# Kernel tuning notes

Hardware: AMD Instinct MI355X
Metric: run time of the kernel (lower is better)

The kernel has to match this reference:

```python
import jax, jax.numpy as jnp
import numpy as np

BS, C, D = 4096, 16384, 128
POS_ALPHA, POS_DELTA = 32.0, 0.1
NEG_ALPHA, NEG_DELTA = 32.0, -0.1


def _normalize(x):
    # F.normalize(x, dim=1)
    return x / jnp.linalg.norm(x, axis=1, keepdims=True)


def _masked_lse(sims, mask, axis, use_max):
    """Faithful port of Criterion.masked_logsumexp (returns per-entry lse and the
    nonzero-entry mask that torch uses to filter before the final mean)."""
    m = sims * mask
    if use_max:
        ref = jnp.max(m, axis=axis, keepdims=True)
    else:
        ref = jnp.min(m, axis=axis, keepdims=True)
    ref = jax.lax.stop_gradient(ref)  # torch: ref_v.detach()
    # torch: nz_entries = max + min of (sims*mask); keep where nonzero
    nz = (jnp.max(m, axis=axis) + jnp.min(m, axis=axis)) != 0
    s = jnp.sum(jnp.exp(sims - ref) * mask, axis=axis)
    lse = jnp.log(jnp.where(nz, s, 1.0)) + jnp.squeeze(ref, axis=axis)
    return lse, nz


def setup_inputs() -> dict:
    key = jax.random.key(0)
    k1, k2, k3 = jax.random.split(key, 3)
    batch = jax.random.normal(k1, (BS, D), dtype=jnp.float32)
    # proxies = randn/proxy_div, init_dev=0 so no max-shift
    proxies = jax.random.normal(k2, (C, D), dtype=jnp.float32) / 8.0
    labels = jax.random.randint(k3, (BS,), 0, C)
    return {"batch": batch, "proxies": proxies, "labels": labels}


def reference(batch, proxies, labels):
    batch = _normalize(batch)          # [BS, D]
    proxies = _normalize(proxies)      # [C, D]

    pos_sims = batch @ proxies[labels].T   # [BS, BS] cosine sims to positive proxies
    sims = batch @ proxies.T               # [BS, C]

    same = (labels[:, None] == labels[None, :]).astype(batch.dtype)              # [BS, BS]
    diff = (labels[:, None] != jnp.arange(C)[None, :]).astype(batch.dtype)       # [BS, C]

    w_pos = -POS_ALPHA * (pos_sims - POS_DELTA)
    w_neg = NEG_ALPHA * (sims - NEG_DELTA)

    # mode='anchor' -> dim=0; cosine -> max=False for pos, max=True for neg
    pos_lse, pos_nz = _masked_lse(w_pos, same, axis=0, use_max=False)
    neg_lse, neg_nz = _masked_lse(w_neg, diff, axis=0, use_max=True)

    # nca_clean=False -> softplus
    pos_s = jax.nn.softplus(pos_lse)
    neg_s = jax.nn.softplus(neg_lse)

    # torch takes mean only over nz entries
    pos_mean = jnp.sum(jnp.where(pos_nz, pos_s, 0.0)) / jnp.maximum(jnp.sum(pos_nz), 1).astype(batch.dtype)
    neg_mean = jnp.sum(jnp.where(neg_nz, neg_s, 0.0)) / jnp.maximum(jnp.sum(neg_nz), 1).astype(batch.dtype)
    return pos_mean + neg_mean
```

## Files before the change

kernel.cpp:

```cpp
#include <hip/hip_runtime.h>
#include <math.h>

#define BS 4096
#define C_CLS 16384
#define D 128
#define NS 8
#define NR 8
#define KE 46.16624130844683f
#define POS_C 4.616624130844683f
#define LN2 0.69314718055994531f
#define CORR_BLOCKS 256
#define NEG_BLOCKS 512

typedef __attribute__((ext_vector_type(8))) short short8;
typedef __attribute__((ext_vector_type(4))) float f32x4;

__device__ inline float bf2f(unsigned short h) {
    return __uint_as_float(((unsigned)h) << 16);
}
__device__ inline unsigned short f2bf(float f) {
    unsigned u = __float_as_uint(f);
    u += 0x7FFF + ((u >> 16) & 1);
    return (unsigned short)(u >> 16);
}
__device__ inline float fastexp2(float x) {
    return __int_as_float((int)fmaf(x, 8388608.0f, 1064866816.0f));
}
__device__ inline float softplus(float x) {
    return fmaxf(x, 0.0f) + log1pf(__expf(-fabsf(x)));
}
__device__ inline void gload16(const void* g, void* l) {
    __builtin_amdgcn_global_load_lds((const __attribute__((address_space(1))) void*)g,
                                     (__attribute__((address_space(3))) void*)l, 16, 0, 0);
}
__device__ inline unsigned fenc(float f) {
    unsigned u = __float_as_uint(f);
    return (u & 0x80000000u) ? ~u : (u | 0x80000000u);
}
__device__ inline float fdec(unsigned k) {
    return (k & 0x80000000u) ? __uint_as_float(k ^ 0x80000000u) : __uint_as_float(~k);
}

__global__ __launch_bounds__(256) void normalize_all(const float* __restrict__ batch,
                                                     const float* __restrict__ proxies,
                                                     short* __restrict__ bbf,
                                                     short* __restrict__ pbf,
                                                     float* __restrict__ acc,
                                                     float* __restrict__ negSub,
                                                     float* __restrict__ posSum,
                                                     float* __restrict__ posCnt,
                                                     unsigned* __restrict__ posMaxK,
                                                     unsigned* __restrict__ posMinK,
                                                     int* __restrict__ counter) {
    const int sub = threadIdx.x >> 5;
    const int lane32 = threadIdx.x & 31;
    const int row = blockIdx.x * 8 + sub;
    const bool isb = row < BS;
    const float* src = isb ? batch : proxies;
    short* dst = isb ? bbf : pbf;
    const int r = isb ? row : row - BS;
    const float sc = isb ? 1.0f : KE;

    float4 v = ((const float4*)(src + (size_t)r * D))[lane32];
    float ss = v.x * v.x + v.y * v.y + v.z * v.z + v.w * v.w;
#pragma unroll
    for (int off = 16; off; off >>= 1) ss += __shfl_xor(ss, off);
    float inv = rsqrtf(ss) * sc;
    ushort4 o;
    o.x = f2bf(v.x * inv);
    o.y = f2bf(v.y * inv);
    o.z = f2bf(v.z * inv);
    o.w = f2bf(v.w * inv);
    ((ushort4*)(dst + (size_t)r * D))[lane32] = o;

    const int bid = blockIdx.x, t = threadIdx.x;
    if (bid < 64) negSub[bid * 256 + t] = 0.0f;
    else if (bid < 128) posSum[(bid - 64) * 256 + t] = 0.0f;
    else if (bid < 192) posCnt[(bid - 128) * 256 + t] = 0.0f;
    else if (bid < 256) posMaxK[(bid - 192) * 256 + t] = 0u;
    else if (bid < 320) posMinK[(bid - 256) * 256 + t] = 0xFFFFFFFFu;
    if (bid == 0 && t == 0) *counter = 0;
}

__global__ __launch_bounds__(256, 1) void mm_all(const short* __restrict__ pbf,
                                                 const short* __restrict__ bbf,
                                                 const int* __restrict__ labels,
                                                 float* __restrict__ S,
                                                 float* __restrict__ negSub,
                                                 float* __restrict__ posSum,
                                                 float* __restrict__ posCnt,
                                                 unsigned* __restrict__ posMaxK,
                                                 unsigned* __restrict__ posMinK) {
    __shared__ short8 frag[3][16 * 64];

    const int bid = blockIdx.x;
    const int tid = threadIdx.x;
    const int w = tid >> 6, lane = tid & 63, l16 = lane & 15, g = lane >> 4;

    if (bid < CORR_BLOCKS) {
        const int ibase = bid * 16 + w * 4;
        int lab[4];
        float d[4];
#pragma unroll
        for (int r = 0; r < 4; r++) {
            const int i = ibase + r;
            lab[r] = labels[i];
            ushort2 av = ((const ushort2*)(bbf + (size_t)i * D))[lane];
            ushort2 pv = ((const ushort2*)(pbf + (size_t)lab[r] * D))[lane];
            d[r] = bf2f(av.x) * bf2f(pv.x) + bf2f(av.y) * bf2f(pv.y);
        }
#pragma unroll
        for (int off = 32; off; off >>= 1)
#pragma unroll
            for (int r = 0; r < 4; r++) d[r] += __shfl_xor(d[r], off);

        if (lane == 0) {
#pragma unroll
            for (int r = 0; r < 4; r++) {
                atomicAdd(&negSub[lab[r]], fastexp2(d[r]));
                atomicAdd(&posSum[lab[r]], fastexp2(POS_C - d[r]));
                atomicAdd(&posCnt[lab[r]], 1.0f);
                unsigned k = fenc(fmaf(d[r], -LN2, 3.2f));
                atomicMax(&posMaxK[lab[r]], k);
                atomicMin(&posMinK[lab[r]], k);
            }
        }
        return;
    }

    const int n = bid - CORR_BLOCKS;
    const int pg = (n & 7) * 8 + ((n >> 3) & 7);
    const int sp = n >> 6;
    const int wbase = pg * 256 + w * 64;

    short8 a[4][4];
#pragma unroll
    for (int pt = 0; pt < 4; pt++)
#pragma unroll
        for (int kk = 0; kk < 4; kk++)
            a[pt][kk] = *(const short8*)(pbf + (size_t)(wbase + pt * 16 + l16) * D + kk * 32 + g * 8);
#pragma unroll
    for (int pt = 0; pt < 4; pt++)
#pragma unroll
        for (int kk = 0; kk < 4; kk++)
            asm volatile("" : "+v"(a[pt][kk]));

    float s[4][4];
#pragma unroll
    for (int pt = 0; pt < 4; pt++)
#pragma unroll
        for (int r = 0; r < 4; r++) s[pt][r] = 0.0f;

    const int ibeg = sp * (BS / NS);
    const short* srcbase = bbf + (size_t)(ibeg + w * 16 + l16) * D + g * 8;

#define STAGE(rr)                                                            \
    {                                                                        \
        const short* sn_ = srcbase + (size_t)(rr) * 64 * D;                  \
        _Pragma("unroll") for (int kk = 0; kk < 4; kk++)                     \
            gload16(sn_ + kk * 32, &frag[(rr) % 3][(w * 4 + kk) * 64]);      \
    }

    STAGE(0)
    STAGE(1)

    for (int rnd = 0; rnd < NR; rnd++) {
        if (rnd < NR - 1)
            asm volatile("s_waitcnt vmcnt(4)" ::: "memory");
        else
            asm volatile("s_waitcnt vmcnt(0)" ::: "memory");
        __builtin_amdgcn_s_barrier();

        const short8* fb = &frag[rnd % 3][0];
#pragma unroll
        for (int bth = 0; bth < 2; bth++) {
            f32x4 pacc[2][4];
#pragma unroll
            for (int bi = 0; bi < 2; bi++)
#pragma unroll
                for (int pt = 0; pt < 4; pt++)
                    pacc[bi][pt] = (f32x4){0.0f, 0.0f, 0.0f, 0.0f};
#pragma unroll
            for (int bi = 0; bi < 2; bi++) {
                const int bt = bth * 2 + bi;
                short8 b[4];
#pragma unroll
                for (int kk = 0; kk < 4; kk++) b[kk] = fb[(bt * 4 + kk) * 64 + lane];
#pragma unroll
                for (int pt = 0; pt < 4; pt++)
#pragma unroll
                    for (int kk = 0; kk < 4; kk++)
                        pacc[bi][pt] = __builtin_amdgcn_mfma_f32_16x16x32_bf16(
                            a[pt][kk], b[kk], pacc[bi][pt], 0, 0, 0);
            }
#pragma unroll
            for (int bi = 0; bi < 2; bi++)
#pragma unroll
                for (int pt = 0; pt < 4; pt++)
#pragma unroll
                    for (int r = 0; r < 4; r++)
                        s[pt][r] += fastexp2(pacc[bi][pt][r]);
        }

        if (rnd + 2 < NR) STAGE(rnd + 2)
    }
#undef STAGE

#pragma unroll
    for (int off = 1; off < 16; off <<= 1)
#pragma unroll
        for (int pt = 0; pt < 4; pt++)
#pragma unroll
            for (int r = 0; r < 4; r++) s[pt][r] += __shfl_xor(s[pt][r], off);

    if (l16 == 0) {
#pragma unroll
        for (int pt = 0; pt < 4; pt++)
#pragma unroll
            for (int r = 0; r < 4; r++) {
                int row = wbase + pt * 16 + g * 4 + r;
                S[(size_t)sp * C_CLS + row] = s[pt][r];
            }
    }
}

__global__ __launch_bounds__(256) void final_reduce(const float* __restrict__ S,
                                                    const float* __restrict__ negSub,
                                                    const int* __restrict__ labels,
                                                    const float* __restrict__ posSum,
                                                    const float* __restrict__ posCnt,
                                                    const unsigned* __restrict__ posMaxK,
                                                    const unsigned* __restrict__ posMinK,
                                                    float* __restrict__ acc,
                                                    int* __restrict__ counter,
                                                    float* __restrict__ out) {
    const int n = blockIdx.x * 256 + threadIdx.x;
    float add = 0.0f, cnt = 0.0f;
    int slot;
    if (n < C_CLS) {
        slot = 2;
        float s = 0.0f;
#pragma unroll
        for (int p = 0; p < NS; p++) s += S[(size_t)p * C_CLS + n];
        s = fmaxf(s - negSub[n], 1e-30f);
        add = softplus(logf(s) + 3.2f);
        cnt = 1.0f;
    } else {
        slot = 0;
        const int j = n - C_CLS;
        const int lab = labels[j];
        float s = posSum[lab], c = posCnt[lab];
        float mxw = fdec(posMaxK[lab]), mnw = fdec(posMinK[lab]);
        float maxm = (c < (float)BS) ? fmaxf(mxw, 0.0f) : mxw;
        float minm = (c < (float)BS) ? fminf(mnw, 0.0f) : mnw;
        bool nz = (maxm + minm) != 0.0f;
        if (nz) {
            add = softplus(logf(s));
            cnt = 1.0f;
        }
    }
#pragma unroll
    for (int off = 32; off; off >>= 1) {
        add += __shfl_xor(add, off);
        cnt += __shfl_xor(cnt, off);
    }
    if ((threadIdx.x & 63) == 0) {
        atomicAdd(&acc[slot], add);
        atomicAdd(&acc[slot + 1], cnt);
    }

    __shared__ int amLast;
    __threadfence();
    if (threadIdx.x == 0) amLast = (atomicAdd(counter, 1) == (int)gridDim.x - 1);
    __syncthreads();
    if (amLast && threadIdx.x == 0) {
        __threadfence();
        out[0] = acc[0] / fmaxf(acc[1], 1.0f) + acc[2] / fmaxf(acc[3], 1.0f);
    }
}

extern "C" void kernel_launch(void* const* d_in, const int* in_sizes, int n_in,
                              void* d_out, int out_size, void* d_ws, size_t ws_size,
                              hipStream_t stream) {
    const float* batch = (const float*)d_in[0];
    const float* proxies = (const float*)d_in[1];
    const int* labels = (const int*)d_in[2];
    float* out = (float*)d_out;

    char* ws = (char*)d_ws;
    float* acc = (float*)ws;
    int* counter = (int*)(ws + 64);
    short* bbf = (short*)(ws + 256);
    short* pbf = (short*)(ws + 256 + (size_t)BS * D * 2);
    char* p = ws + 256 + (size_t)(BS + C_CLS) * D * 2;
    float* negS = (float*)p;          p += (size_t)C_CLS * NS * 4;
    float* negSub = (float*)p;        p += (size_t)C_CLS * 4;
    float* posSum = (float*)p;        p += (size_t)C_CLS * 4;
    float* posCnt = (float*)p;        p += (size_t)C_CLS * 4;
    unsigned* posMaxK = (unsigned*)p; p += (size_t)C_CLS * 4;
    unsigned* posMinK = (unsigned*)p;

    normalize_all<<<(BS + C_CLS) / 8, 256, 0, stream>>>(batch, proxies, bbf, pbf, acc,
                                                        negSub, posSum, posCnt, posMaxK,
                                                        posMinK, counter);
    mm_all<<<CORR_BLOCKS + NEG_BLOCKS, 256, 0, stream>>>(pbf, bbf, labels, negS, negSub,
                                                         posSum, posCnt, posMaxK, posMinK);
    final_reduce<<<(C_CLS + BS) / 256, 256, 0, stream>>>(negS, negSub, labels, posSum,
                                                         posCnt, posMaxK, posMinK,
                                                         acc, counter, out);
}
```

Measured before the change: 44.52 us.

## Warp-specialize mm_all into MFMA producer waves and exp consumer waves

The negative-similarity kernel now runs with 512 threads per block. Four waves compute MFMA tiles and write accumulators to a shared LDS buffer. The other four waves read them back and do the exp2 accumulation, so the transcendental work can overlap with the next tile's matrix multiply. The cost is two extra block barriers per tile and an LDS round trip for every accumulator. The new launch bounds of (512, 4) also tighten the per-thread register budget, which risks spilling the 64-VGPR A fragment.

```diff
diff --git a/kernel.cpp b/kernel.cpp
--- a/kernel.cpp
+++ b/kernel.cpp
@@ -82,7 +82,7 @@
     if (bid == 0 && t == 0) *counter = 0;
 }
 
-__global__ __launch_bounds__(256, 1) void mm_all(const short* __restrict__ pbf,
+__global__ __launch_bounds__(512, 4) void mm_all(const short* __restrict__ pbf,
                                                  const short* __restrict__ bbf,
                                                  const int* __restrict__ labels,
                                                  float* __restrict__ S,
@@ -92,17 +92,18 @@
                                                  unsigned* __restrict__ posMaxK,
                                                  unsigned* __restrict__ posMinK) {
     __shared__ short8 frag[3][16 * 64];
+    __shared__ f32x4 accbuf[16 * 64];
 
     const int bid = blockIdx.x;
     const int tid = threadIdx.x;
     const int w = tid >> 6, lane = tid & 63, l16 = lane & 15, g = lane >> 4;
 
     if (bid < CORR_BLOCKS) {
-        const int ibase = bid * 16 + w * 4;
-        int lab[4];
-        float d[4];
-#pragma unroll
-        for (int r = 0; r < 4; r++) {
+        const int ibase = bid * 16 + w * 2;
+        int lab[2];
+        float d[2];
+#pragma unroll
+        for (int r = 0; r < 2; r++) {
             const int i = ibase + r;
             lab[r] = labels[i];
             ushort2 av = ((const ushort2*)(bbf + (size_t)i * D))[lane];
@@ -112,11 +113,11 @@
 #pragma unroll
         for (int off = 32; off; off >>= 1)
 #pragma unroll
-            for (int r = 0; r < 4; r++) d[r] += __shfl_xor(d[r], off);
+            for (int r = 0; r < 2; r++) d[r] += __shfl_xor(d[r], off);
 
         if (lane == 0) {
 #pragma unroll
-            for (int r = 0; r < 4; r++) {
+            for (int r = 0; r < 2; r++) {
                 atomicAdd(&negSub[lab[r]], fastexp2(d[r]));
                 atomicAdd(&posSum[lab[r]], fastexp2(POS_C - d[r]));
                 atomicAdd(&posCnt[lab[r]], 1.0f);
@@ -131,96 +132,107 @@
     const int n = bid - CORR_BLOCKS;
     const int pg = (n & 7) * 8 + ((n >> 3) & 7);
     const int sp = n >> 6;
-    const int wbase = pg * 256 + w * 64;
-
-    short8 a[4][4];
-#pragma unroll
-    for (int pt = 0; pt < 4; pt++)
-#pragma unroll
-        for (int kk = 0; kk < 4; kk++)
-            a[pt][kk] = *(const short8*)(pbf + (size_t)(wbase + pt * 16 + l16) * D + kk * 32 + g * 8);
-#pragma unroll
-    for (int pt = 0; pt < 4; pt++)
-#pragma unroll
-        for (int kk = 0; kk < 4; kk++)
-            asm volatile("" : "+v"(a[pt][kk]));
-
-    float s[4][4];
-#pragma unroll
-    for (int pt = 0; pt < 4; pt++)
-#pragma unroll
-        for (int r = 0; r < 4; r++) s[pt][r] = 0.0f;
+    const bool prod = (w < 4);
+    const int pw = w & 3;
+    const int wbase = pg * 256 + pw * 64;
 
     const int ibeg = sp * (BS / NS);
-    const short* srcbase = bbf + (size_t)(ibeg + w * 16 + l16) * D + g * 8;
+    const short* srcbase = bbf + (size_t)(ibeg + pw * 16 + l16) * D + g * 8;
 
 #define STAGE(rr)                                                            \
     {                                                                        \
         const short* sn_ = srcbase + (size_t)(rr) * 64 * D;                  \
         _Pragma("unroll") for (int kk = 0; kk < 4; kk++)                     \
-            gload16(sn_ + kk * 32, &frag[(rr) % 3][(w * 4 + kk) * 64]);      \
-    }
-
-    STAGE(0)
-    STAGE(1)
+            gload16(sn_ + kk * 32, &frag[(rr) % 3][(pw * 4 + kk) * 64]);     \
+    }
+
+    short8 a[4][4];
+    float s[4][4];
+    if (prod) {
+#pragma unroll
+        for (int pt = 0; pt < 4; pt++)
+#pragma unroll
+            for (int kk = 0; kk < 4; kk++)
+                a[pt][kk] = *(const short8*)(pbf + (size_t)(wbase + pt * 16 + l16) * D + kk * 32 + g * 8);
+#pragma unroll
+        for (int pt = 0; pt < 4; pt++)
+#pragma unroll
+            for (int kk = 0; kk < 4; kk++)
+                asm volatile("" : "+v"(a[pt][kk]));
+        STAGE(0)
+        STAGE(1)
+    } else {
+#pragma unroll
+        for (int pt = 0; pt < 4; pt++)
+#pragma unroll
+            for (int r = 0; r < 4; r++) s[pt][r] = 0.0f;
+    }
 
     for (int rnd = 0; rnd < NR; rnd++) {
-        if (rnd < NR - 1)
-            asm volatile("s_waitcnt vmcnt(4)" ::: "memory");
-        else
-            asm volatile("s_waitcnt vmcnt(0)" ::: "memory");
+        if (prod) {
+            if (rnd < NR - 1)
+                asm volatile("s_waitcnt vmcnt(4)" ::: "memory");
+            else
+                asm volatile("s_waitcnt vmcnt(0)" ::: "memory");
+        }
         __builtin_amdgcn_s_barrier();
 
         const short8* fb = &frag[rnd % 3][0];
 #pragma unroll
-        for (int bth = 0; bth < 2; bth++) {
-            f32x4 pacc[2][4];
-#pragma unroll
-            for (int bi = 0; bi < 2; bi++)
+        for (int bt = 0; bt < 4; bt++) {
+            f32x4 pacc[4];
+            if (prod) {
+                short8 b[4];
+#pragma unroll
+                for (int kk = 0; kk < 4; kk++) b[kk] = fb[(bt * 4 + kk) * 64 + lane];
+#pragma unroll
+                for (int pt = 0; pt < 4; pt++) {
+                    pacc[pt] = (f32x4){0.0f, 0.0f, 0.0f, 0.0f};
+#pragma unroll
+                    for (int kk = 0; kk < 4; kk++)
+                        pacc[pt] = __builtin_amdgcn_mfma_f32_16x16x32_bf16(
+                            a[pt][kk], b[kk], pacc[pt], 0, 0, 0);
+                }
+            }
+            __builtin_amdgcn_s_barrier();
+            if (prod) {
 #pragma unroll
                 for (int pt = 0; pt < 4; pt++)
-                    pacc[bi][pt] = (f32x4){0.0f, 0.0f, 0.0f, 0.0f};
-#pragma unroll
-            for (int bi = 0; bi < 2; bi++) {
-                const int bt = bth * 2 + bi;
-                short8 b[4];
-#pragma unroll
-                for (int kk = 0; kk < 4; kk++) b[kk] = fb[(bt * 4 + kk) * 64 + lane];
-#pragma unroll
-                for (int pt = 0; pt < 4; pt++)
-#pragma unroll
-                    for (int kk = 0; kk < 4; kk++)
-                        pacc[bi][pt] = __builtin_amdgcn_mfma_f32_16x16x32_bf16(
-                            a[pt][kk], b[kk], pacc[bi][pt], 0, 0, 0);
+                    accbuf[(pw * 4 + pt) * 64 + lane] = pacc[pt];
+                asm volatile("s_waitcnt lgkmcnt(0)" ::: "memory");
+                __builtin_amdgcn_sched_barrier(0);
             }
-#pragma unroll
-            for (int bi = 0; bi < 2; bi++)
-#pragma unroll
-                for (int pt = 0; pt < 4; pt++)
-#pragma unroll
-                    for (int r = 0; r < 4; r++)
-                        s[pt][r] += fastexp2(pacc[bi][pt][r]);
-        }
-
-        if (rnd + 2 < NR) STAGE(rnd + 2)
+            __builtin_amdgcn_s_barrier();
+            if (!prod) {
+#pragma unroll
+                for (int pt = 0; pt < 4; pt++) {
+                    f32x4 v = accbuf[(pw * 4 + pt) * 64 + lane];
+#pragma unroll
+                    for (int r = 0; r < 4; r++) s[pt][r] += fastexp2(v[r]);
+                }
+            }
+        }
+        if (prod && rnd + 2 < NR) STAGE(rnd + 2)
     }
 #undef STAGE
 
-#pragma unroll
-    for (int off = 1; off < 16; off <<= 1)
-#pragma unroll
-        for (int pt = 0; pt < 4; pt++)
-#pragma unroll
-            for (int r = 0; r < 4; r++) s[pt][r] += __shfl_xor(s[pt][r], off);
-
-    if (l16 == 0) {
-#pragma unroll
-        for (int pt = 0; pt < 4; pt++)
-#pragma unroll
-            for (int r = 0; r < 4; r++) {
-                int row = wbase + pt * 16 + g * 4 + r;
-                S[(size_t)sp * C_CLS + row] = s[pt][r];
-            }
+    if (!prod) {
+#pragma unroll
+        for (int off = 1; off < 16; off <<= 1)
+#pragma unroll
+            for (int pt = 0; pt < 4; pt++)
+#pragma unroll
+                for (int r = 0; r < 4; r++) s[pt][r] += __shfl_xor(s[pt][r], off);
+
+        if (l16 == 0) {
+#pragma unroll
+            for (int pt = 0; pt < 4; pt++)
+#pragma unroll
+                for (int r = 0; r < 4; r++) {
+                    int row = wbase + pt * 16 + g * 4 + r;
+                    S[(size_t)sp * C_CLS + row] = s[pt][r];
+                }
+        }
     }
 }
 
@@ -303,7 +315,7 @@
     normalize_all<<<(BS + C_CLS) / 8, 256, 0, stream>>>(batch, proxies, bbf, pbf, acc,
                                                         negSub, posSum, posCnt, posMaxK,
                                                         posMinK, counter);
-    mm_all<<<CORR_BLOCKS + NEG_BLOCKS, 256, 0, stream>>>(pbf, bbf, labels, negS, negSub,
+    mm_all<<<CORR_BLOCKS + NEG_BLOCKS, 512, 0, stream>>>(pbf, bbf, labels, negS, negSub,
                                                          posSum, posCnt, posMaxK, posMinK);
     final_reduce<<<(C_CLS + BS) / 256, 256, 0, stream>>>(negS, negSub, labels, posSum,
                                                          posCnt, posMaxK, posMinK,
```

New measurement: 51.10 us. 14.8% more time.
